# Optimization experiments

Hardware: AMD Instinct MI355X
Metric: run time of the kernel (lower is better)

Reference implementation:

```python
import jax, jax.numpy as jnp
import numpy as np

HEADS = 4
OUT_CH = 32
IN_CH = 128
HC = HEADS * OUT_CH  # 128
N = 100000
G = 1000
E = 1600000
EG = 16000
NEG_SLOPE = 0.2


def gat_conv(x, edge_index, W, att_src, att_dst, bias):
    """PyG-style GATConv (concat heads, self-loops, leaky_relu 0.2, eval mode)."""
    n = x.shape[0]
    loop = jnp.arange(n)
    src = jnp.concatenate([edge_index[0], loop])
    dst = jnp.concatenate([edge_index[1], loop])
    h = (x @ W).reshape(n, HEADS, OUT_CH)            # [n,H,C]
    a_src = (h * att_src).sum(-1)                    # [n,H]
    a_dst = (h * att_dst).sum(-1)                    # [n,H]
    e = jax.nn.leaky_relu(a_src[src] + a_dst[dst], NEG_SLOPE)  # [e,H]
    m = jax.ops.segment_max(e, dst, num_segments=n)
    ex = jnp.exp(e - m[dst])
    s = jax.ops.segment_sum(ex, dst, num_segments=n)
    alpha = ex / (s[dst] + 1e-16)
    out = jax.ops.segment_sum(alpha[:, :, None] * h[src], dst, num_segments=n)
    return out.reshape(n, HC) + bias


def setup_inputs() -> dict:
    key = jax.random.key(0)
    ks = jax.random.split(key, 16)
    inv = 1.0 / np.sqrt(IN_CH)
    invh = 1.0 / np.sqrt(HC)
    return {
        "x": jax.random.normal(ks[0], (N, IN_CH), jnp.float32),
        "x_g": jax.random.normal(ks[1], (G, IN_CH), jnp.float32),
        "edge_index": jax.random.randint(ks[2], (2, E), 0, N, jnp.int32),
        "edge_index_g": jax.random.randint(ks[3], (2, EG), 0, G, jnp.int32),
        "node_group": jax.random.randint(ks[4], (N,), 0, G, jnp.int32),
        "W1": jax.random.normal(ks[5], (IN_CH, HC), jnp.float32) * inv,
        "att_src1": jax.random.normal(ks[6], (HEADS, OUT_CH), jnp.float32) * invh,
        "att_dst1": jax.random.normal(ks[7], (HEADS, OUT_CH), jnp.float32) * invh,
        "bias1": jnp.zeros((HC,), jnp.float32),
        "W2": jax.random.normal(ks[8], (IN_CH, HC), jnp.float32) * inv,
        "att_src2": jax.random.normal(ks[9], (HEADS, OUT_CH), jnp.float32) * invh,
        "att_dst2": jax.random.normal(ks[10], (HEADS, OUT_CH), jnp.float32) * invh,
        "bias2": jnp.zeros((HC,), jnp.float32),
        "W_fc": jax.random.normal(ks[11], (HC, OUT_CH), jnp.float32) * invh,
        "b_fc": jnp.zeros((OUT_CH,), jnp.float32),
    }


def reference(x, x_g, edge_index, edge_index_g, node_group,
              W1, att_src1, att_dst1, bias1,
              W2, att_src2, att_dst2, bias2, W_fc, b_fc):
    x_out = gat_conv(x, edge_index, W1, att_src1, att_dst1, bias1)      # [N,HC]
    x_g_out = gat_conv(x_g, edge_index_g, W2, att_src2, att_dst2, bias2)  # [G,HC]

    # mean of adjacent group features per group (segment mean over group edges)
    adj_sum = jax.ops.segment_sum(x_g_out[edge_index_g[1]], edge_index_g[0], num_segments=G)
    cnt = jax.ops.segment_sum(jnp.ones((edge_index_g.shape[1],), x_g_out.dtype),
                              edge_index_g[0], num_segments=G)
    adj_mean = adj_sum / jnp.maximum(cnt, 1.0)[:, None]                  # [G,HC]

    gf = x_g_out[node_group]          # per-node own-group feature   [N,HC]
    af = adj_mean[node_group]         # per-node adjacent-group mean [N,HC]
    imp_g = jnp.einsum('nc,nc->n', x_out, gf)
    imp_a = jnp.einsum('nc,nc->n', x_out, af)
    upd = x_out + imp_g[:, None] * gf + imp_a[:, None] * af
    out = upd @ W_fc + b_fc
    return out, x_g_out
```

## Files before the change

kernel.cpp:

```cpp
#include <hip/hip_runtime.h>

__host__ __device__ static inline int imin(int a, int b) { return a < b ? a : b; }

__device__ __forceinline__ float lrelu(float v) { return v > 0.f ? v : 0.2f * v; }

#define GR 8
__global__ __launch_bounds__(256) void gemm128(const float* __restrict__ X,
                                               const float* __restrict__ W,
                                               const float* __restrict__ att_s,
                                               const float* __restrict__ att_d,
                                               float* __restrict__ H,
                                               float* __restrict__ asrc,
                                               float* __restrict__ adst, int n) {
  __shared__ float Wt[128 * 128];
  __shared__ float Xl[4][GR * 128];
  const int tid = threadIdx.x;
  for (int i = tid; i < 4096; i += 256) {
    int c = i >> 5;
    int j0 = (i & 31) * 4;
    float4 w = ((const float4*)W)[i];
    float wv[4] = {w.x, w.y, w.z, w.w};
    int cu = c >> 2, cr = c & 3;
#pragma unroll
    for (int k = 0; k < 4; ++k) {
      int j = j0 + k;
      Wt[j * 128 + 4 * (cu ^ (j & 31)) + cr] = wv[k];
    }
  }
  __syncthreads();

  const int wave = tid >> 6, lane = tid & 63;
  const float as_l = att_s[lane], as_h = att_s[lane + 64];
  const float ad_l = att_d[lane], ad_h = att_d[lane + 64];
  const int sw = lane & 31;
  const float4* wt0 = (const float4*)&Wt[lane * 128];
  const float4* wt1 = (const float4*)&Wt[(lane + 64) * 128];
  float* xw = &Xl[wave][0];

  const int nb = (n + 31) >> 5;
  for (int tb = blockIdx.x; tb < nb; tb += gridDim.x) {
    const int rbase = tb * 32 + wave * GR;
#pragma unroll
    for (int rr = 0; rr < GR; ++rr) {
      int r = rbase + rr;
      float2 v = make_float2(0.f, 0.f);
      if (r < n) v = ((const float2*)(X + (size_t)r * 128))[lane];
      ((float2*)(xw + rr * 128))[lane] = v;
    }
    float a0[GR], a1[GR];
#pragma unroll
    for (int rr = 0; rr < GR; ++rr) {
      a0[rr] = 0.f;
      a1[rr] = 0.f;
    }
#pragma unroll 2
    for (int u = 0; u < 32; ++u) {
      float4 w0 = wt0[u ^ sw];
      float4 w1 = wt1[u ^ sw];
#pragma unroll
      for (int rr = 0; rr < GR; ++rr) {
        float4 xv = *((const float4*)(xw + rr * 128 + 4 * u));
        a0[rr] = fmaf(xv.x, w0.x, a0[rr]);
        a0[rr] = fmaf(xv.y, w0.y, a0[rr]);
        a0[rr] = fmaf(xv.z, w0.z, a0[rr]);
        a0[rr] = fmaf(xv.w, w0.w, a0[rr]);
        a1[rr] = fmaf(xv.x, w1.x, a1[rr]);
        a1[rr] = fmaf(xv.y, w1.y, a1[rr]);
        a1[rr] = fmaf(xv.z, w1.z, a1[rr]);
        a1[rr] = fmaf(xv.w, w1.w, a1[rr]);
      }
    }
#pragma unroll
    for (int rr = 0; rr < GR; ++rr) {
      int r = rbase + rr;
      if (r < n) {
        H[(size_t)r * 128 + lane] = a0[rr];
        H[(size_t)r * 128 + lane + 64] = a1[rr];
        float ps0 = a0[rr] * as_l, pd0 = a0[rr] * ad_l;
        float ps1 = a1[rr] * as_h, pd1 = a1[rr] * ad_h;
#pragma unroll
        for (int m = 16; m >= 1; m >>= 1) {
          ps0 += __shfl_xor(ps0, m);
          pd0 += __shfl_xor(pd0, m);
          ps1 += __shfl_xor(ps1, m);
          pd1 += __shfl_xor(pd1, m);
        }
        if (lane == 0) {
          asrc[(size_t)r * 4 + 0] = ps0;
          adst[(size_t)r * 4 + 0] = pd0;
          asrc[(size_t)r * 4 + 2] = ps1;
          adst[(size_t)r * 4 + 2] = pd1;
        } else if (lane == 32) {
          asrc[(size_t)r * 4 + 1] = ps0;
          adst[(size_t)r * 4 + 1] = pd0;
          asrc[(size_t)r * 4 + 3] = ps1;
          adst[(size_t)r * 4 + 3] = pd1;
        }
      }
    }
  }
}

__global__ __launch_bounds__(256) void count_deg(const int* __restrict__ dst, int ne,
                                                 int* __restrict__ deg) {
  int i = blockIdx.x * 256 + threadIdx.x;
  if (i < ne) atomicAdd(&deg[dst[i]], 1);
}

__global__ __launch_bounds__(256) void scan_part1(const int* __restrict__ in, int n,
                                                  int* __restrict__ bsum) {
  int base = blockIdx.x * 4096 + threadIdx.x * 16;
  int s = 0;
  if (base + 16 <= n) {
    const int4* p = (const int4*)(in + base);
#pragma unroll
    for (int k = 0; k < 4; ++k) {
      int4 v = p[k];
      s += v.x + v.y + v.z + v.w;
    }
  } else {
    for (int k = 0; k < 16; ++k) {
      int i = base + k;
      if (i < n) s += in[i];
    }
  }
#pragma unroll
  for (int o = 1; o < 64; o <<= 1) s += __shfl_xor(s, o);
  __shared__ int ws[4];
  int wave = threadIdx.x >> 6, lane = threadIdx.x & 63;
  if (lane == 0) ws[wave] = s;
  __syncthreads();
  if (threadIdx.x == 0) bsum[blockIdx.x] = ws[0] + ws[1] + ws[2] + ws[3];
}

__global__ __launch_bounds__(256) void scan_part2(int* __restrict__ bsum, int nb,
                                                  int* __restrict__ off, int n) {
  __shared__ int sm[256];
  int tid = threadIdx.x;
  int v = (tid < nb) ? bsum[tid] : 0;
  sm[tid] = v;
  __syncthreads();
  int x = v;
  for (int o = 1; o < 256; o <<= 1) {
    int t = (tid >= o) ? sm[tid - o] : 0;
    __syncthreads();
    x += t;
    sm[tid] = x;
    __syncthreads();
  }
  if (tid < nb) bsum[tid] = x - v;
  if (tid == 0) off[n] = sm[255];
}

__global__ __launch_bounds__(256) void scan_part3(const int* __restrict__ in, int n,
                                                  const int* __restrict__ bsum,
                                                  int* __restrict__ out) {
  int tid = threadIdx.x;
  int base = blockIdx.x * 4096 + tid * 16;
  int vals[16];
  if (base + 16 <= n) {
    const int4* p = (const int4*)(in + base);
#pragma unroll
    for (int k = 0; k < 4; ++k) {
      int4 v = p[k];
      vals[4 * k] = v.x;
      vals[4 * k + 1] = v.y;
      vals[4 * k + 2] = v.z;
      vals[4 * k + 3] = v.w;
    }
  } else {
#pragma unroll
    for (int k = 0; k < 16; ++k) {
      int i = base + k;
      vals[k] = (i < n) ? in[i] : 0;
    }
  }
  int tsum = 0;
#pragma unroll
  for (int k = 0; k < 16; ++k) tsum += vals[k];
  int lane = tid & 63, wave = tid >> 6;
  int inc = tsum;
#pragma unroll
  for (int o = 1; o < 64; o <<= 1) {
    int t = __shfl_up(inc, o);
    if (lane >= o) inc += t;
  }
  int exc = inc - tsum;
  __shared__ int ws[4];
  if (lane == 63) ws[wave] = inc;
  __syncthreads();
  int woff = 0;
  for (int w = 0; w < wave; ++w) woff += ws[w];
  int off0 = bsum[blockIdx.x] + woff + exc;
  int run = 0;
#pragma unroll
  for (int k = 0; k < 16; ++k) {
    int i = base + k;
    if (i < n) out[i] = off0 + run;
    run += vals[k];
  }
}

__global__ __launch_bounds__(256) void fill_csr(const int* __restrict__ src,
                                                const int* __restrict__ dst, int ne,
                                                const int* __restrict__ off,
                                                int* __restrict__ cur,
                                                int* __restrict__ csr) {
  int i = blockIdx.x * 256 + threadIdx.x;
  if (i < ne) {
    int d = dst[i];
    int p = atomicAdd(&cur[d], 1);
    csr[off[d] + p] = src[i];
  }
}

__global__ __launch_bounds__(256) void gat_aggregate(
    const float* __restrict__ H, const float* __restrict__ asrc,
    const float* __restrict__ adst, const int* __restrict__ off,
    const int* __restrict__ csr, const float* __restrict__ bias,
    float* __restrict__ out, int n) {
  __shared__ float4 exl[4][64];
  int gw = (blockIdx.x * 256 + threadIdx.x) >> 6;
  if (gw >= n) return;
  int wave = (threadIdx.x >> 6), lane = threadIdx.x & 63;
  int n0 = off[gw];
  int deg = off[gw + 1] - n0;

  float4 ad = ((const float4*)adst)[gw];
  int c0 = lane * 2;
  int hd = lane >> 4;
  float4 s4 = make_float4(0.f, 0.f, 0.f, 0.f);
  float acc0 = 0.f, acc1 = 0.f;
  const float* exw = (const float*)&exl[wave][0];

  for (int base = 0; base < deg; base += 64) {
    int idx = base + lane;
    bool v = idx < deg;
    int sr = v ? csr[n0 + idx] : 0;
    float4 ex = make_float4(0.f, 0.f, 0.f, 0.f);
    if (v) {
      float4 as = ((const float4*)asrc)[sr];
      ex.x = __expf(lrelu(as.x + ad.x));
      ex.y = __expf(lrelu(as.y + ad.y));
      ex.z = __expf(lrelu(as.z + ad.z));
      ex.w = __expf(lrelu(as.w + ad.w));
      s4.x += ex.x;
      s4.y += ex.y;
      s4.z += ex.z;
      s4.w += ex.w;
    }
    exl[wave][lane] = ex;
    int cnt = imin(64, deg - base);
    int j = 0;
    for (; j + 4 <= cnt; j += 4) {
      int sj0 = __shfl(sr, j);
      int sj1 = __shfl(sr, j + 1);
      int sj2 = __shfl(sr, j + 2);
      int sj3 = __shfl(sr, j + 3);
      float2 h0 = ((const float2*)(H + (size_t)sj0 * 128))[lane];
      float2 h1 = ((const float2*)(H + (size_t)sj1 * 128))[lane];
      float2 h2 = ((const float2*)(H + (size_t)sj2 * 128))[lane];
      float2 h3 = ((const float2*)(H + (size_t)sj3 * 128))[lane];
      float e0 = exw[(j + 0) * 4 + hd];
      float e1 = exw[(j + 1) * 4 + hd];
      float e2 = exw[(j + 2) * 4 + hd];
      float e3 = exw[(j + 3) * 4 + hd];
      acc0 = fmaf(e0, h0.x, acc0);
      acc1 = fmaf(e0, h0.y, acc1);
      acc0 = fmaf(e1, h1.x, acc0);
      acc1 = fmaf(e1, h1.y, acc1);
      acc0 = fmaf(e2, h2.x, acc0);
      acc1 = fmaf(e2, h2.y, acc1);
      acc0 = fmaf(e3, h3.x, acc0);
      acc1 = fmaf(e3, h3.y, acc1);
    }
    for (; j < cnt; ++j) {
      int srj = __shfl(sr, j);
      float exh = exw[j * 4 + hd];
      float2 hv = ((const float2*)(H + (size_t)srj * 128))[lane];
      acc0 = fmaf(exh, hv.x, acc0);
      acc1 = fmaf(exh, hv.y, acc1);
    }
  }
#pragma unroll
  for (int o = 1; o < 64; o <<= 1) {
    s4.x += __shfl_xor(s4.x, o);
    s4.y += __shfl_xor(s4.y, o);
    s4.z += __shfl_xor(s4.z, o);
    s4.w += __shfl_xor(s4.w, o);
  }
  float4 asn = ((const float4*)asrc)[gw];
  float4 exs;
  exs.x = __expf(lrelu(asn.x + ad.x));
  exs.y = __expf(lrelu(asn.y + ad.y));
  exs.z = __expf(lrelu(asn.z + ad.z));
  exs.w = __expf(lrelu(asn.w + ad.w));
  s4.x += exs.x;
  s4.y += exs.y;
  s4.z += exs.z;
  s4.w += exs.w;
  float s_h = (hd == 0) ? s4.x : (hd == 1) ? s4.y : (hd == 2) ? s4.z : s4.w;
  float e_h = (hd == 0) ? exs.x : (hd == 1) ? exs.y : (hd == 2) ? exs.z : exs.w;
  float2 hs = ((const float2*)(H + (size_t)gw * 128))[lane];
  acc0 = fmaf(e_h, hs.x, acc0);
  acc1 = fmaf(e_h, hs.y, acc1);
  float inv = 1.f / (s_h + 1e-16f);
  out[(size_t)gw * 128 + c0] = acc0 * inv + bias[c0];
  out[(size_t)gw * 128 + c0 + 1] = acc1 * inv + bias[c0 + 1];
}

__global__ __launch_bounds__(256) void adj_accum(const int* __restrict__ gsrc,
                                                 const int* __restrict__ gdst,
                                                 const float* __restrict__ xgout,
                                                 float* __restrict__ adj,
                                                 float* __restrict__ cnt, int ne) {
  int idx = blockIdx.x * 256 + threadIdx.x;
  if (idx >= ne * 64) return;
  int e = idx >> 6;
  int l = idx & 63;
  int gs = gsrc[e], gd = gdst[e];
  float2 v = ((const float2*)(xgout + (size_t)gd * 128))[l];
  atomicAdd(&adj[(size_t)gs * 128 + 2 * l], v.x);
  atomicAdd(&adj[(size_t)gs * 128 + 2 * l + 1], v.y);
  if (l == 0) atomicAdd(&cnt[gs], 1.0f);
}

__global__ __launch_bounds__(256) void final_fuse(
    const float* __restrict__ xout, const float* __restrict__ xgout,
    const float* __restrict__ adjm, const float* __restrict__ cnt,
    const int* __restrict__ ngrp, const float* __restrict__ Wfc,
    const float* __restrict__ bfc, float* __restrict__ out, int n) {
  __shared__ float Wl[128 * 32];
  __shared__ float up[4][128];
  int tid = threadIdx.x;
  for (int i = tid; i < 1024; i += 256)
    ((float4*)Wl)[i] = ((const float4*)Wfc)[i];
  __syncthreads();

  int wave = tid >> 6, lane = tid & 63;
  int tw = gridDim.x * 4;
  for (int node = blockIdx.x * 4 + wave; node < n; node += tw) {
    int g = ngrp[node];
    float2 xo = ((const float2*)(xout + (size_t)node * 128))[lane];
    float2 gf = ((const float2*)(xgout + (size_t)g * 128))[lane];
    float2 af = ((const float2*)(adjm + (size_t)g * 128))[lane];
    float cinv = 1.f / fmaxf(cnt[g], 1.0f);
    af.x *= cinv;
    af.y *= cinv;
    float pg = xo.x * gf.x + xo.y * gf.y;
    float pa = xo.x * af.x + xo.y * af.y;
#pragma unroll
    for (int o = 1; o < 64; o <<= 1) {
      pg += __shfl_xor(pg, o);
      pa += __shfl_xor(pa, o);
    }
    float u0 = xo.x + pg * gf.x + pa * af.x;
    float u1 = xo.y + pg * gf.y + pa * af.y;
    up[wave][lane * 2] = u0;
    up[wave][lane * 2 + 1] = u1;
    int j = lane & 31;
    int ch = (lane >> 5) * 64;
    float acc = 0.f;
#pragma unroll 8
    for (int cc = 0; cc < 64; ++cc)
      acc = fmaf(up[wave][ch + cc], Wl[(ch + cc) * 32 + j], acc);
    acc += __shfl_xor(acc, 32);
    if (lane < 32) out[(size_t)node * 32 + j] = acc + bfc[j];
  }
}

extern "C" void kernel_launch(void* const* d_in, const int* in_sizes, int n_in,
                              void* d_out, int out_size, void* d_ws, size_t ws_size,
                              hipStream_t stream) {
  const float* x = (const float*)d_in[0];
  const float* xg = (const float*)d_in[1];
  const int* ei = (const int*)d_in[2];
  const int* eig = (const int*)d_in[3];
  const int* ngrp = (const int*)d_in[4];
  const float* W1 = (const float*)d_in[5];
  const float* as1 = (const float*)d_in[6];
  const float* ad1 = (const float*)d_in[7];
  const float* b1 = (const float*)d_in[8];
  const float* W2 = (const float*)d_in[9];
  const float* as2 = (const float*)d_in[10];
  const float* ad2 = (const float*)d_in[11];
  const float* b2 = (const float*)d_in[12];
  const float* Wfc = (const float*)d_in[13];
  const float* bfc = (const float*)d_in[14];

  const int N = in_sizes[0] / 128;
  const int G = in_sizes[1] / 128;
  const int E = in_sizes[2] / 2;
  const int EG = in_sizes[3] / 2;

  char* p = (char*)d_ws;
  auto carve = [&](size_t bytes) {
    void* r = (void*)p;
    p += (bytes + 255) & ~(size_t)255;
    return r;
  };
  float* h1 = (float*)carve((size_t)N * 128 * 4);
  float* xout = (float*)carve((size_t)N * 128 * 4);
  float* asrc1 = (float*)carve((size_t)N * 16);
  float* adst1 = (float*)carve((size_t)N * 16);
  int* off1 = (int*)carve((size_t)(N + 1) * 4);
  int* deg1 = (int*)carve((size_t)N * 4);
  int* csr1 = (int*)carve((size_t)E * 4);
  float* h2 = (float*)carve((size_t)G * 128 * 4);
  float* asrc2 = (float*)carve((size_t)G * 16);
  float* adst2 = (float*)carve((size_t)G * 16);
  int* off2 = (int*)carve((size_t)(G + 1) * 4);
  int* deg2 = (int*)carve((size_t)G * 4);
  int* csr2 = (int*)carve((size_t)EG * 4);
  float* adjm = (float*)carve((size_t)G * 128 * 4);
  float* cnt = (float*)carve((size_t)G * 4);
  int* bsum1 = (int*)carve(256 * 4);
  int* bsum2 = (int*)carve(256 * 4);

  float* outN = (float*)d_out;
  float* xgout = (float*)d_out + (size_t)N * 32;

  const int* src1 = ei;
  const int* dst1 = ei + E;
  const int* srcg = eig;
  const int* dstg = eig + EG;

  hipMemsetAsync(deg1, 0, (size_t)N * 4, stream);
  hipMemsetAsync(deg2, 0, (size_t)G * 4, stream);
  hipMemsetAsync(adjm, 0, (size_t)G * 128 * 4, stream);
  hipMemsetAsync(cnt, 0, (size_t)G * 4, stream);

  const int nbt1 = (N + 31) / 32;
  const int nbt2 = (G + 31) / 32;
  gemm128<<<imin(nbt1, 512), 256, 0, stream>>>(x, W1, as1, ad1, h1, asrc1, adst1, N);
  gemm128<<<imin(nbt2, 512), 256, 0, stream>>>(xg, W2, as2, ad2, h2, asrc2, adst2, G);
  count_deg<<<(E + 255) / 256, 256, 0, stream>>>(dst1, E, deg1);
  count_deg<<<(EG + 255) / 256, 256, 0, stream>>>(dstg, EG, deg2);

  const int nb1 = (N + 4095) / 4096;
  const int nb2 = (G + 4095) / 4096;
  scan_part1<<<nb1, 256, 0, stream>>>(deg1, N, bsum1);
  scan_part2<<<1, 256, 0, stream>>>(bsum1, nb1, off1, N);
  scan_part3<<<nb1, 256, 0, stream>>>(deg1, N, bsum1, off1);
  scan_part1<<<nb2, 256, 0, stream>>>(deg2, G, bsum2);
  scan_part2<<<1, 256, 0, stream>>>(bsum2, nb2, off2, G);
  scan_part3<<<nb2, 256, 0, stream>>>(deg2, G, bsum2, off2);

  hipMemsetAsync(deg1, 0, (size_t)N * 4, stream);
  hipMemsetAsync(deg2, 0, (size_t)G * 4, stream);
  fill_csr<<<(E + 255) / 256, 256, 0, stream>>>(src1, dst1, E, off1, deg1, csr1);
  fill_csr<<<(EG + 255) / 256, 256, 0, stream>>>(srcg, dstg, EG, off2, deg2, csr2);
  gat_aggregate<<<(N + 3) / 4, 256, 0, stream>>>(h1, asrc1, adst1, off1, csr1, b1, xout, N);
  gat_aggregate<<<(G + 3) / 4, 256, 0, stream>>>(h2, asrc2, adst2, off2, csr2, b2, xgout, G);
  adj_accum<<<(EG * 64 + 255) / 256, 256, 0, stream>>>(srcg, dstg, xgout, adjm, cnt, EG);
  final_fuse<<<2048, 256, 0, stream>>>(xout, xgout, adjm, cnt, ngrp, Wfc, bfc, outN, N);
}
```

Baseline: 623.9 us.

## Batch graph preprocessing launches, half-wave GAT aggregation, CSR-based adjacency mean

Merges the degree-count, three scan stages and CSR fill for both graphs (plus a new source-keyed group CSR) into single multi-segment kernels, and replaces the separate memsets with one. gat_aggregate now assigns each destination node to half a wave, using float4 loads and LDS-staged source indices instead of shuffles. The atomic adj_accum is replaced by a gather-based adj_sum over a source-sorted CSR that also folds in the mean division. Together these aim to cut launch overhead and atomics and to improve memory access width in the aggregation, at the cost of an extra CSR build and less per-node parallelism for high-degree nodes.

```diff
diff --git a/kernel.cpp b/kernel.cpp
--- a/kernel.cpp
+++ b/kernel.cpp
@@ -101,15 +101,24 @@
   }
 }
 
-__global__ __launch_bounds__(256) void count_deg(const int* __restrict__ dst, int ne,
-                                                 int* __restrict__ deg) {
+__global__ __launch_bounds__(256) void count3(const int* __restrict__ d1, int n1,
+                                              int* __restrict__ c1,
+                                              const int* __restrict__ d2, int n2,
+                                              int* __restrict__ c2,
+                                              const int* __restrict__ d3, int n3,
+                                              int* __restrict__ c3) {
   int i = blockIdx.x * 256 + threadIdx.x;
-  if (i < ne) atomicAdd(&deg[dst[i]], 1);
-}
-
-__global__ __launch_bounds__(256) void scan_part1(const int* __restrict__ in, int n,
-                                                  int* __restrict__ bsum) {
-  int base = blockIdx.x * 4096 + threadIdx.x * 16;
+  if (i < n1) atomicAdd(&c1[d1[i]], 1);
+  int i2 = i - n1;
+  if (i2 >= 0 && i2 < n2) atomicAdd(&c2[d2[i2]], 1);
+  int i3 = i2 - n2;
+  if (i3 >= 0 && i3 < n3) atomicAdd(&c3[d3[i3]], 1);
+}
+
+__device__ __forceinline__ void scan1_block(const int* __restrict__ in, int n,
+                                            int* __restrict__ bsum, int blk,
+                                            int* ws) {
+  int base = blk * 4096 + threadIdx.x * 16;
   int s = 0;
   if (base + 16 <= n) {
     const int4* p = (const int4*)(in + base);
@@ -126,16 +135,26 @@
   }
 #pragma unroll
   for (int o = 1; o < 64; o <<= 1) s += __shfl_xor(s, o);
-  __shared__ int ws[4];
   int wave = threadIdx.x >> 6, lane = threadIdx.x & 63;
   if (lane == 0) ws[wave] = s;
   __syncthreads();
-  if (threadIdx.x == 0) bsum[blockIdx.x] = ws[0] + ws[1] + ws[2] + ws[3];
-}
-
-__global__ __launch_bounds__(256) void scan_part2(int* __restrict__ bsum, int nb,
-                                                  int* __restrict__ off, int n) {
-  __shared__ int sm[256];
+  if (threadIdx.x == 0) bsum[blk] = ws[0] + ws[1] + ws[2] + ws[3];
+}
+
+__global__ __launch_bounds__(256) void scan_part1m(
+    const int* __restrict__ i1, int n1, int* __restrict__ b1,
+    const int* __restrict__ i2, int n2, int* __restrict__ b2,
+    const int* __restrict__ i3, int n3, int* __restrict__ b3) {
+  __shared__ int ws[4];
+  int nb1 = (n1 + 4095) / 4096, nb2 = (n2 + 4095) / 4096;
+  int b = blockIdx.x;
+  if (b < nb1) scan1_block(i1, n1, b1, b, ws);
+  else if (b < nb1 + nb2) scan1_block(i2, n2, b2, b - nb1, ws);
+  else scan1_block(i3, n3, b3, b - nb1 - nb2, ws);
+}
+
+__device__ __forceinline__ void scan2_block(int* __restrict__ bsum, int nb,
+                                            int* __restrict__ off, int n, int* sm) {
   int tid = threadIdx.x;
   int v = (tid < nb) ? bsum[tid] : 0;
   sm[tid] = v;
@@ -150,13 +169,27 @@
   }
   if (tid < nb) bsum[tid] = x - v;
   if (tid == 0) off[n] = sm[255];
-}
-
-__global__ __launch_bounds__(256) void scan_part3(const int* __restrict__ in, int n,
-                                                  const int* __restrict__ bsum,
-                                                  int* __restrict__ out) {
+  __syncthreads();
+}
+
+__global__ __launch_bounds__(256) void scan_part2m(int* __restrict__ b1, int nb1,
+                                                   int* __restrict__ o1, int n1,
+                                                   int* __restrict__ b2, int nb2,
+                                                   int* __restrict__ o2, int n2,
+                                                   int* __restrict__ b3, int nb3,
+                                                   int* __restrict__ o3, int n3) {
+  __shared__ int sm[256];
+  scan2_block(b1, nb1, o1, n1, sm);
+  scan2_block(b2, nb2, o2, n2, sm);
+  scan2_block(b3, nb3, o3, n3, sm);
+}
+
+__device__ __forceinline__ void scan3_block(const int* __restrict__ in, int n,
+                                            const int* __restrict__ bsum,
+                                            int* __restrict__ out, int blk,
+                                            int* ws) {
   int tid = threadIdx.x;
-  int base = blockIdx.x * 4096 + tid * 16;
+  int base = blk * 4096 + tid * 16;
   int vals[16];
   if (base + 16 <= n) {
     const int4* p = (const int4*)(in + base);
@@ -186,12 +219,11 @@
     if (lane >= o) inc += t;
   }
   int exc = inc - tsum;
-  __shared__ int ws[4];
   if (lane == 63) ws[wave] = inc;
   __syncthreads();
   int woff = 0;
   for (int w = 0; w < wave; ++w) woff += ws[w];
-  int off0 = bsum[blockIdx.x] + woff + exc;
+  int off0 = bsum[blk] + woff + exc;
   int run = 0;
 #pragma unroll
   for (int k = 0; k < 16; ++k) {
@@ -201,16 +233,42 @@
   }
 }
 
-__global__ __launch_bounds__(256) void fill_csr(const int* __restrict__ src,
-                                                const int* __restrict__ dst, int ne,
-                                                const int* __restrict__ off,
-                                                int* __restrict__ cur,
-                                                int* __restrict__ csr) {
+__global__ __launch_bounds__(256) void scan_part3m(
+    const int* __restrict__ i1, int n1, const int* __restrict__ b1, int* __restrict__ o1,
+    const int* __restrict__ i2, int n2, const int* __restrict__ b2, int* __restrict__ o2,
+    const int* __restrict__ i3, int n3, const int* __restrict__ b3, int* __restrict__ o3) {
+  __shared__ int ws[4];
+  int nb1 = (n1 + 4095) / 4096, nb2 = (n2 + 4095) / 4096;
+  int b = blockIdx.x;
+  if (b < nb1) scan3_block(i1, n1, b1, o1, b, ws);
+  else if (b < nb1 + nb2) scan3_block(i2, n2, b2, o2, b - nb1, ws);
+  else scan3_block(i3, n3, b3, o3, b - nb1 - nb2, ws);
+}
+
+__global__ __launch_bounds__(256) void fill3(
+    const int* __restrict__ s1, const int* __restrict__ d1, int n1,
+    const int* __restrict__ o1, int* __restrict__ c1, int* __restrict__ r1,
+    const int* __restrict__ s2, const int* __restrict__ d2, int n2,
+    const int* __restrict__ o2, int* __restrict__ c2, int* __restrict__ r2,
+    const int* __restrict__ s3, const int* __restrict__ d3, int n3,
+    const int* __restrict__ o3, int* __restrict__ c3, int* __restrict__ r3) {
   int i = blockIdx.x * 256 + threadIdx.x;
-  if (i < ne) {
-    int d = dst[i];
-    int p = atomicAdd(&cur[d], 1);
-    csr[off[d] + p] = src[i];
+  if (i < n1) {
+    int d = d1[i];
+    int p = atomicAdd(&c1[d], 1);
+    r1[o1[d] + p] = s1[i];
+  }
+  int i2 = i - n1;
+  if (i2 >= 0 && i2 < n2) {
+    int d = d2[i2];
+    int p = atomicAdd(&c2[d], 1);
+    r2[o2[d] + p] = s2[i2];
+  }
+  int i3 = i2 - n2;
+  if (i3 >= 0 && i3 < n3) {
+    int d = d3[i3];
+    int p = atomicAdd(&c3[d], 1);
+    r3[o3[d] + p] = s3[i3];
   }
 }
 
@@ -219,22 +277,28 @@
     const float* __restrict__ adst, const int* __restrict__ off,
     const int* __restrict__ csr, const float* __restrict__ bias,
     float* __restrict__ out, int n) {
-  __shared__ float4 exl[4][64];
-  int gw = (blockIdx.x * 256 + threadIdx.x) >> 6;
-  if (gw >= n) return;
-  int wave = (threadIdx.x >> 6), lane = threadIdx.x & 63;
-  int n0 = off[gw];
-  int deg = off[gw + 1] - n0;
-
-  float4 ad = ((const float4*)adst)[gw];
-  int c0 = lane * 2;
-  int hd = lane >> 4;
+  __shared__ float exl[4][256];
+  __shared__ int srl[4][64];
+  int wid = (blockIdx.x * 256 + threadIdx.x) >> 6;
+  int wave = threadIdx.x >> 6, lane = threadIdx.x & 63;
+  int hw = lane >> 5, lid = lane & 31;
+  int gw = wid * 2 + hw;
+  bool active = gw < n;
+  int n0 = 0, deg = 0;
+  if (active) {
+    n0 = off[gw];
+    deg = off[gw + 1] - n0;
+  }
+  float4 ad = make_float4(0.f, 0.f, 0.f, 0.f);
+  if (active) ad = ((const float4*)adst)[gw];
+  int hd = lid >> 3;
   float4 s4 = make_float4(0.f, 0.f, 0.f, 0.f);
-  float acc0 = 0.f, acc1 = 0.f;
-  const float* exw = (const float*)&exl[wave][0];
-
-  for (int base = 0; base < deg; base += 64) {
-    int idx = base + lane;
+  float4 acc = make_float4(0.f, 0.f, 0.f, 0.f);
+  float* exw = &exl[wave][hw * 128];
+  int* srw = &srl[wave][hw * 32];
+
+  for (int base = 0; base < deg; base += 32) {
+    int idx = base + lid;
     bool v = idx < deg;
     int sr = v ? csr[n0 + idx] : 0;
     float4 ex = make_float4(0.f, 0.f, 0.f, 0.f);
@@ -249,87 +313,109 @@
       s4.z += ex.z;
       s4.w += ex.w;
     }
-    exl[wave][lane] = ex;
-    int cnt = imin(64, deg - base);
+    ((float4*)exw)[lid] = ex;
+    srw[lid] = sr;
+    int cnt = imin(32, deg - base);
     int j = 0;
     for (; j + 4 <= cnt; j += 4) {
-      int sj0 = __shfl(sr, j);
-      int sj1 = __shfl(sr, j + 1);
-      int sj2 = __shfl(sr, j + 2);
-      int sj3 = __shfl(sr, j + 3);
-      float2 h0 = ((const float2*)(H + (size_t)sj0 * 128))[lane];
-      float2 h1 = ((const float2*)(H + (size_t)sj1 * 128))[lane];
-      float2 h2 = ((const float2*)(H + (size_t)sj2 * 128))[lane];
-      float2 h3 = ((const float2*)(H + (size_t)sj3 * 128))[lane];
+      int s0 = srw[j], s1 = srw[j + 1], s2 = srw[j + 2], s3 = srw[j + 3];
+      float4 h0 = ((const float4*)(H + (size_t)s0 * 128))[lid];
+      float4 h1 = ((const float4*)(H + (size_t)s1 * 128))[lid];
+      float4 h2 = ((const float4*)(H + (size_t)s2 * 128))[lid];
+      float4 h3 = ((const float4*)(H + (size_t)s3 * 128))[lid];
       float e0 = exw[(j + 0) * 4 + hd];
       float e1 = exw[(j + 1) * 4 + hd];
       float e2 = exw[(j + 2) * 4 + hd];
       float e3 = exw[(j + 3) * 4 + hd];
-      acc0 = fmaf(e0, h0.x, acc0);
-      acc1 = fmaf(e0, h0.y, acc1);
-      acc0 = fmaf(e1, h1.x, acc0);
-      acc1 = fmaf(e1, h1.y, acc1);
-      acc0 = fmaf(e2, h2.x, acc0);
-      acc1 = fmaf(e2, h2.y, acc1);
-      acc0 = fmaf(e3, h3.x, acc0);
-      acc1 = fmaf(e3, h3.y, acc1);
+      acc.x = fmaf(e0, h0.x, acc.x);
+      acc.y = fmaf(e0, h0.y, acc.y);
+      acc.z = fmaf(e0, h0.z, acc.z);
+      acc.w = fmaf(e0, h0.w, acc.w);
+      acc.x = fmaf(e1, h1.x, acc.x);
+      acc.y = fmaf(e1, h1.y, acc.y);
+      acc.z = fmaf(e1, h1.z, acc.z);
+      acc.w = fmaf(e1, h1.w, acc.w);
+      acc.x = fmaf(e2, h2.x, acc.x);
+      acc.y = fmaf(e2, h2.y, acc.y);
+      acc.z = fmaf(e2, h2.z, acc.z);
+      acc.w = fmaf(e2, h2.w, acc.w);
+      acc.x = fmaf(e3, h3.x, acc.x);
+      acc.y = fmaf(e3, h3.y, acc.y);
+      acc.z = fmaf(e3, h3.z, acc.z);
+      acc.w = fmaf(e3, h3.w, acc.w);
     }
     for (; j < cnt; ++j) {
-      int srj = __shfl(sr, j);
-      float exh = exw[j * 4 + hd];
-      float2 hv = ((const float2*)(H + (size_t)srj * 128))[lane];
-      acc0 = fmaf(exh, hv.x, acc0);
-      acc1 = fmaf(exh, hv.y, acc1);
-    }
-  }
-#pragma unroll
-  for (int o = 1; o < 64; o <<= 1) {
+      int sj = srw[j];
+      float4 hv = ((const float4*)(H + (size_t)sj * 128))[lid];
+      float ej = exw[j * 4 + hd];
+      acc.x = fmaf(ej, hv.x, acc.x);
+      acc.y = fmaf(ej, hv.y, acc.y);
+      acc.z = fmaf(ej, hv.z, acc.z);
+      acc.w = fmaf(ej, hv.w, acc.w);
+    }
+  }
+#pragma unroll
+  for (int o = 1; o < 32; o <<= 1) {
     s4.x += __shfl_xor(s4.x, o);
     s4.y += __shfl_xor(s4.y, o);
     s4.z += __shfl_xor(s4.z, o);
     s4.w += __shfl_xor(s4.w, o);
   }
-  float4 asn = ((const float4*)asrc)[gw];
-  float4 exs;
-  exs.x = __expf(lrelu(asn.x + ad.x));
-  exs.y = __expf(lrelu(asn.y + ad.y));
-  exs.z = __expf(lrelu(asn.z + ad.z));
-  exs.w = __expf(lrelu(asn.w + ad.w));
-  s4.x += exs.x;
-  s4.y += exs.y;
-  s4.z += exs.z;
-  s4.w += exs.w;
-  float s_h = (hd == 0) ? s4.x : (hd == 1) ? s4.y : (hd == 2) ? s4.z : s4.w;
-  float e_h = (hd == 0) ? exs.x : (hd == 1) ? exs.y : (hd == 2) ? exs.z : exs.w;
-  float2 hs = ((const float2*)(H + (size_t)gw * 128))[lane];
-  acc0 = fmaf(e_h, hs.x, acc0);
-  acc1 = fmaf(e_h, hs.y, acc1);
-  float inv = 1.f / (s_h + 1e-16f);
-  out[(size_t)gw * 128 + c0] = acc0 * inv + bias[c0];
-  out[(size_t)gw * 128 + c0 + 1] = acc1 * inv + bias[c0 + 1];
-}
-
-__global__ __launch_bounds__(256) void adj_accum(const int* __restrict__ gsrc,
-                                                 const int* __restrict__ gdst,
-                                                 const float* __restrict__ xgout,
-                                                 float* __restrict__ adj,
-                                                 float* __restrict__ cnt, int ne) {
-  int idx = blockIdx.x * 256 + threadIdx.x;
-  if (idx >= ne * 64) return;
-  int e = idx >> 6;
-  int l = idx & 63;
-  int gs = gsrc[e], gd = gdst[e];
-  float2 v = ((const float2*)(xgout + (size_t)gd * 128))[l];
-  atomicAdd(&adj[(size_t)gs * 128 + 2 * l], v.x);
-  atomicAdd(&adj[(size_t)gs * 128 + 2 * l + 1], v.y);
-  if (l == 0) atomicAdd(&cnt[gs], 1.0f);
+  if (active) {
+    float4 asn = ((const float4*)asrc)[gw];
+    float4 exs;
+    exs.x = __expf(lrelu(asn.x + ad.x));
+    exs.y = __expf(lrelu(asn.y + ad.y));
+    exs.z = __expf(lrelu(asn.z + ad.z));
+    exs.w = __expf(lrelu(asn.w + ad.w));
+    s4.x += exs.x;
+    s4.y += exs.y;
+    s4.z += exs.z;
+    s4.w += exs.w;
+    float s_h = (hd == 0) ? s4.x : (hd == 1) ? s4.y : (hd == 2) ? s4.z : s4.w;
+    float e_h = (hd == 0) ? exs.x : (hd == 1) ? exs.y : (hd == 2) ? exs.z : exs.w;
+    float4 hs = ((const float4*)(H + (size_t)gw * 128))[lid];
+    acc.x = fmaf(e_h, hs.x, acc.x);
+    acc.y = fmaf(e_h, hs.y, acc.y);
+    acc.z = fmaf(e_h, hs.z, acc.z);
+    acc.w = fmaf(e_h, hs.w, acc.w);
+    float inv = 1.f / (s_h + 1e-16f);
+    float4 b = ((const float4*)bias)[lid];
+    float4 o4;
+    o4.x = acc.x * inv + b.x;
+    o4.y = acc.y * inv + b.y;
+    o4.z = acc.z * inv + b.z;
+    o4.w = acc.w * inv + b.w;
+    ((float4*)(out + (size_t)gw * 128))[lid] = o4;
+  }
+}
+
+__global__ __launch_bounds__(256) void adj_sum(const float* __restrict__ xgout,
+                                               const int* __restrict__ offs,
+                                               const int* __restrict__ csrs,
+                                               float* __restrict__ adjm, int g_cnt) {
+  int g = (blockIdx.x * 256 + threadIdx.x) >> 6;
+  if (g >= g_cnt) return;
+  int lane = threadIdx.x & 63;
+  int o0 = offs[g];
+  int dg = offs[g + 1] - o0;
+  float2 acc = make_float2(0.f, 0.f);
+  for (int j = 0; j < dg; ++j) {
+    int d = csrs[o0 + j];
+    float2 v = ((const float2*)(xgout + (size_t)d * 128))[lane];
+    acc.x += v.x;
+    acc.y += v.y;
+  }
+  float inv = 1.f / fmaxf((float)dg, 1.f);
+  adjm[(size_t)g * 128 + lane * 2] = acc.x * inv;
+  adjm[(size_t)g * 128 + lane * 2 + 1] = acc.y * inv;
 }
 
 __global__ __launch_bounds__(256) void final_fuse(
     const float* __restrict__ xout, const float* __restrict__ xgout,
-    const float* __restrict__ adjm, const float* __restrict__ cnt,
-    const int* __restrict__ ngrp, const float* __restrict__ Wfc,
-    const float* __restrict__ bfc, float* __restrict__ out, int n) {
+    const float* __restrict__ adjm, const int* __restrict__ ngrp,
+    const float* __restrict__ Wfc, const float* __restrict__ bfc,
+    float* __restrict__ out, int n) {
   __shared__ float Wl[128 * 32];
   __shared__ float up[4][128];
   int tid = threadIdx.x;
@@ -344,9 +430,6 @@
     float2 xo = ((const float2*)(xout + (size_t)node * 128))[lane];
     float2 gf = ((const float2*)(xgout + (size_t)g * 128))[lane];
     float2 af = ((const float2*)(adjm + (size_t)g * 128))[lane];
-    float cinv = 1.f / fmaxf(cnt[g], 1.0f);
-    af.x *= cinv;
-    af.y *= cinv;
     float pg = xo.x * gf.x + xo.y * gf.y;
     float pa = xo.x * af.x + xo.y * af.y;
 #pragma unroll
@@ -403,19 +486,27 @@
   float* xout = (float*)carve((size_t)N * 128 * 4);
   float* asrc1 = (float*)carve((size_t)N * 16);
   float* adst1 = (float*)carve((size_t)N * 16);
-  int* off1 = (int*)carve((size_t)(N + 1) * 4);
-  int* deg1 = (int*)carve((size_t)N * 4);
-  int* csr1 = (int*)carve((size_t)E * 4);
   float* h2 = (float*)carve((size_t)G * 128 * 4);
   float* asrc2 = (float*)carve((size_t)G * 16);
   float* adst2 = (float*)carve((size_t)G * 16);
+  float* adjm = (float*)carve((size_t)G * 128 * 4);
+  int* off1 = (int*)carve((size_t)(N + 1) * 4);
   int* off2 = (int*)carve((size_t)(G + 1) * 4);
-  int* deg2 = (int*)carve((size_t)G * 4);
+  int* off2s = (int*)carve((size_t)(G + 1) * 4);
+  int* csr1 = (int*)carve((size_t)E * 4);
   int* csr2 = (int*)carve((size_t)EG * 4);
-  float* adjm = (float*)carve((size_t)G * 128 * 4);
-  float* cnt = (float*)carve((size_t)G * 4);
+  int* csr2s = (int*)carve((size_t)EG * 4);
   int* bsum1 = (int*)carve(256 * 4);
   int* bsum2 = (int*)carve(256 * 4);
+  int* bsum3 = (int*)carve(256 * 4);
+  char* z0 = p;
+  int* deg1 = (int*)carve((size_t)N * 4);
+  int* deg2 = (int*)carve((size_t)G * 4);
+  int* deg2s = (int*)carve((size_t)G * 4);
+  int* cur1 = (int*)carve((size_t)N * 4);
+  int* cur2 = (int*)carve((size_t)G * 4);
+  int* cur2s = (int*)carve((size_t)G * 4);
+  size_t zbytes = (size_t)(p - z0);
 
   float* outN = (float*)d_out;
   float* xgout = (float*)d_out + (size_t)N * 32;
@@ -425,33 +516,35 @@
   const int* srcg = eig;
   const int* dstg = eig + EG;
 
-  hipMemsetAsync(deg1, 0, (size_t)N * 4, stream);
-  hipMemsetAsync(deg2, 0, (size_t)G * 4, stream);
-  hipMemsetAsync(adjm, 0, (size_t)G * 128 * 4, stream);
-  hipMemsetAsync(cnt, 0, (size_t)G * 4, stream);
+  hipMemsetAsync(z0, 0, zbytes, stream);
 
   const int nbt1 = (N + 31) / 32;
   const int nbt2 = (G + 31) / 32;
   gemm128<<<imin(nbt1, 512), 256, 0, stream>>>(x, W1, as1, ad1, h1, asrc1, adst1, N);
   gemm128<<<imin(nbt2, 512), 256, 0, stream>>>(xg, W2, as2, ad2, h2, asrc2, adst2, G);
-  count_deg<<<(E + 255) / 256, 256, 0, stream>>>(dst1, E, deg1);
-  count_deg<<<(EG + 255) / 256, 256, 0, stream>>>(dstg, EG, deg2);
+
+  count3<<<(E + 2 * EG + 255) / 256, 256, 0, stream>>>(dst1, E, deg1, dstg, EG, deg2,
+                                                       srcg, EG, deg2s);
 
   const int nb1 = (N + 4095) / 4096;
   const int nb2 = (G + 4095) / 4096;
-  scan_part1<<<nb1, 256, 0, stream>>>(deg1, N, bsum1);
-  scan_part2<<<1, 256, 0, stream>>>(bsum1, nb1, off1, N);
-  scan_part3<<<nb1, 256, 0, stream>>>(deg1, N, bsum1, off1);
-  scan_part1<<<nb2, 256, 0, stream>>>(deg2, G, bsum2);
-  scan_part2<<<1, 256, 0, stream>>>(bsum2, nb2, off2, G);
-  scan_part3<<<nb2, 256, 0, stream>>>(deg2, G, bsum2, off2);
-
-  hipMemsetAsync(deg1, 0, (size_t)N * 4, stream);
-  hipMemsetAsync(deg2, 0, (size_t)G * 4, stream);
-  fill_csr<<<(E + 255) / 256, 256, 0, stream>>>(src1, dst1, E, off1, deg1, csr1);
-  fill_csr<<<(EG + 255) / 256, 256, 0, stream>>>(srcg, dstg, EG, off2, deg2, csr2);
-  gat_aggregate<<<(N + 3) / 4, 256, 0, stream>>>(h1, asrc1, adst1, off1, csr1, b1, xout, N);
-  gat_aggregate<<<(G + 3) / 4, 256, 0, stream>>>(h2, asrc2, adst2, off2, csr2, b2, xgout, G);
-  adj_accum<<<(EG * 64 + 255) / 256, 256, 0, stream>>>(srcg, dstg, xgout, adjm, cnt, EG);
-  final_fuse<<<2048, 256, 0, stream>>>(xout, xgout, adjm, cnt, ngrp, Wfc, bfc, outN, N);
-}
+  const int nb3 = (G + 4095) / 4096;
+  scan_part1m<<<nb1 + nb2 + nb3, 256, 0, stream>>>(deg1, N, bsum1, deg2, G, bsum2,
+                                                   deg2s, G, bsum3);
+  scan_part2m<<<1, 256, 0, stream>>>(bsum1, nb1, off1, N, bsum2, nb2, off2, G,
+                                     bsum3, nb3, off2s, G);
+  scan_part3m<<<nb1 + nb2 + nb3, 256, 0, stream>>>(deg1, N, bsum1, off1, deg2, G,
+                                                   bsum2, off2, deg2s, G, bsum3,
+                                                   off2s);
+
+  fill3<<<(E + 2 * EG + 255) / 256, 256, 0, stream>>>(
+      src1, dst1, E, off1, cur1, csr1, srcg, dstg, EG, off2, cur2, csr2, dstg,
+      srcg, EG, off2s, cur2s, csr2s);
+
+  gat_aggregate<<<(N + 7) / 8, 256, 0, stream>>>(h1, asrc1, adst1, off1, csr1, b1,
+                                                 xout, N);
+  gat_aggregate<<<(G + 7) / 8, 256, 0, stream>>>(h2, asrc2, adst2, off2, csr2, b2,
+                                                 xgout, G);
+  adj_sum<<<(G + 3) / 4, 256, 0, stream>>>(xgout, off2s, csr2s, adjm, G);
+  final_fuse<<<2048, 256, 0, stream>>>(xout, xgout, adjm, ngrp, Wfc, bfc, outN, N);
+}
```

New measurement: 604.5 us. -3.1%, faster.
